# Performance work log

Hardware: AMD Instinct MI355X
Metric: run time of the kernel (lower is better)

## Reference

```python
import jax, jax.numpy as jnp
import numpy as np

V, E, H, T, B, A = 100000, 300, 256, 128, 64, 8
FH, NC = 256, 2
G = 2 * H  # gcn_input_dim = hidden_size * 2


def setup_inputs() -> dict:
    key = jax.random.key(0)
    ks = jax.random.split(key, 28)
    def n(k, shape, scale=0.05):
        return jax.random.normal(k, shape, dtype=jnp.float32) * scale
    return {
        "sentence": jax.random.randint(ks[0], (B, T), 0, V),
        "aspect": jax.random.randint(ks[1], (B, A), 0, V),
        "pos_class": jax.random.randint(ks[2], (B, T), 0, 18),
        "dep_tags": jax.random.randint(ks[3], (B, T), 0, 40),
        "text_len": jax.random.randint(ks[4], (B,), 1, T + 1),
        "aspect_len": jax.random.randint(ks[5], (B,), 1, A + 1),
        "dep_rels": jax.random.randint(ks[6], (B, T), 0, 40),
        "dep_heads": jax.random.randint(ks[7], (B, T), 0, T),
        "aspect_position": jax.random.randint(ks[8], (B, T), 0, 2),
        "dep_dirs": jax.random.randint(ks[9], (B, T), 0, 3),
        # frozen GloVe table
        "glove_emb": jax.random.normal(ks[10], (V, E), dtype=jnp.float32),
        # BiLSTM (1 layer): PyTorch layout, gates ordered i,f,g,o
        "w_ih_f": n(ks[11], (4 * H, E)), "w_hh_f": n(ks[12], (4 * H, H)),
        "b_ih_f": n(ks[13], (4 * H,)), "b_hh_f": n(ks[14], (4 * H,)),
        "w_ih_b": n(ks[15], (4 * H, E)), "w_hh_b": n(ks[16], (4 * H, H)),
        "b_ih_b": n(ks[17], (4 * H,)), "b_hh_b": n(ks[18], (4 * H,)),
        # 'gcn' attention branch: self.gat = nn.Linear(G, G)
        "gat_w": n(ks[19], (G, G)), "gat_b": n(ks[20], (G,)),
        # fcs MLP (num_mlps = 2)
        "fc1_w": n(ks[21], (FH, G)), "fc1_b": n(ks[22], (FH,)),
        "fc2_w": n(ks[23], (FH, FH)), "fc2_b": n(ks[24], (FH,)),
        "fcf_w": n(ks[25], (NC, FH)), "fcf_b": n(ks[26], (NC,)),
    }


def _lstm_dir(x, w_ih, w_hh, b_ih, b_hh, reverse):
    """One direction of a PyTorch-style LSTM. x: (B, T, E) -> (B, T, H)."""
    Bn = x.shape[0]
    Hh = w_hh.shape[1]
    xs = jnp.swapaxes(x, 0, 1)  # (T, B, E)
    if reverse:
        xs = xs[::-1]
    def step(carry, xt):
        h, c = carry
        g = xt @ w_ih.T + b_ih + h @ w_hh.T + b_hh  # (B, 4H)
        i, f, gg, o = jnp.split(g, 4, axis=-1)
        c = jax.nn.sigmoid(f) * c + jax.nn.sigmoid(i) * jnp.tanh(gg)
        h = jax.nn.sigmoid(o) * jnp.tanh(c)
        return (h, c), h
    init = (jnp.zeros((Bn, Hh), x.dtype), jnp.zeros((Bn, Hh), x.dtype))
    _, hs = jax.lax.scan(step, init, xs)
    if reverse:
        hs = hs[::-1]
    return jnp.swapaxes(hs, 0, 1)


def _bilstm(x, w_ih_f, w_hh_f, b_ih_f, b_hh_f, w_ih_b, w_hh_b, b_ih_b, b_hh_b):
    fwd = _lstm_dir(x, w_ih_f, w_hh_f, b_ih_f, b_hh_f, reverse=False)
    bwd = _lstm_dir(x, w_ih_b, w_hh_b, b_ih_b, b_hh_b, reverse=True)
    return jnp.concatenate([fwd, bwd], axis=-1)  # (B, T, 2H)


def reference(sentence, aspect, pos_class, dep_tags, text_len, aspect_len,
              dep_rels, dep_heads, aspect_position, dep_dirs,
              glove_emb, w_ih_f, w_hh_f, b_ih_f, b_hh_f,
              w_ih_b, w_hh_b, b_ih_b, b_hh_b,
              gat_w, gat_b, fc1_w, fc1_b, fc2_w, fc2_b, fcf_w, fcf_b):
    # fmask: per-token validity mask derived from text_len (inputs_to_deprel_adj)
    fmask = (jnp.arange(T)[None, :] < text_len[:, None]).astype(jnp.float32)  # (B, T)
    # embedding lookup (dropout is identity in eval mode)
    feature = glove_emb[sentence]  # (B, T, E)
    # BiLSTM over the sentence. (aspect branch is dead code in the 'gcn' path:
    # aspect_feature is computed but never used, so we omit it.)
    feature = _bilstm(feature, w_ih_f, w_hh_f, b_ih_f, b_hh_f,
                      w_ih_b, w_hh_b, b_ih_b, b_hh_b)  # (B, T, 2H)
    # 'gcn' branch: linear, mask, sum over tokens, relu
    gat_out = feature @ gat_w.T + gat_b           # (B, T, 2H)
    gat_out = gat_out * fmask[:, :, None]
    gat_out = jax.nn.relu(jnp.sum(gat_out, axis=1))  # (B, 2H)
    # fcs MLP + final classifier
    x = jax.nn.relu(gat_out @ fc1_w.T + fc1_b)
    x = jax.nn.relu(x @ fc2_w.T + fc2_b)
    logit = x @ fcf_w.T + fcf_b                    # (B, NC)
    return logit
```

## Files before the change

### kernel.cpp

```cpp
#include <hip/hip_runtime.h>
#include <hip/hip_bf16.h>
#include <math.h>

#define B_  64
#define T_  128
#define E_  300
#define H_  256
#define G4  1024
#define N2  2048
#define GG  512
#define FH_ 256
#define NC_ 2
#define KP  320

typedef __attribute__((ext_vector_type(8))) short short8;
typedef __attribute__((ext_vector_type(4))) float f32x4;
typedef unsigned short ushort_t;
typedef unsigned long long u64;

static __device__ __forceinline__ ushort_t bf16bits(float x) {
    __hip_bfloat16 b = __float2bfloat16(x);
    return __builtin_bit_cast(ushort_t, b);
}
static __device__ __forceinline__ float bf16lo(unsigned v) {
    return __builtin_bit_cast(float, v << 16);
}
static __device__ __forceinline__ float bf16hi(unsigned v) {
    return __builtin_bit_cast(float, v & 0xffff0000u);
}

static __device__ __forceinline__ float sigm_f(float x) {
    return __fdividef(1.f, 1.f + __expf(-x));
}
static __device__ __forceinline__ float tanh_f(float x) {
    return 1.f - __fdividef(2.f, __expf(2.f * x) + 1.f);
}

static __device__ __forceinline__ void ld8_sc0(const u64* p, u64 v[8]) {
    u64 r0, r1, r2, r3, r4, r5, r6, r7;
    asm volatile(
        "global_load_dwordx2 %0, %8, off sc0\n\t"
        "global_load_dwordx2 %1, %8, off offset:8 sc0\n\t"
        "global_load_dwordx2 %2, %8, off offset:16 sc0\n\t"
        "global_load_dwordx2 %3, %8, off offset:24 sc0\n\t"
        "global_load_dwordx2 %4, %8, off offset:32 sc0\n\t"
        "global_load_dwordx2 %5, %8, off offset:40 sc0\n\t"
        "global_load_dwordx2 %6, %8, off offset:48 sc0\n\t"
        "global_load_dwordx2 %7, %8, off offset:56 sc0\n\t"
        "s_waitcnt vmcnt(0)"
        : "=&v"(r0), "=&v"(r1), "=&v"(r2), "=&v"(r3),
          "=&v"(r4), "=&v"(r5), "=&v"(r6), "=&v"(r7)
        : "v"(p)
        : "memory");
    v[0] = r0; v[1] = r1; v[2] = r2; v[3] = r3;
    v[4] = r4; v[5] = r5; v[6] = r6; v[7] = r7;
}

#define OFF_BIAS  262144
#define OFF_WIH   524288
#define OFF_A     1835008
#define OFF_XEMB  2097152
#define OFF_XPROJ 8388608
#define OFF_S     41943040

__global__ __launch_bounds__(256) void k_prep(
    const int*   __restrict__ sentence,
    const float* __restrict__ glove,
    const float* __restrict__ w_ih_f,
    const float* __restrict__ w_ih_b,
    const float* __restrict__ b_ih_f, const float* __restrict__ b_hh_f,
    const float* __restrict__ b_ih_b, const float* __restrict__ b_hh_b,
    u64*         __restrict__ hbufB,
    u64*         __restrict__ hbufA,
    float*       __restrict__ bias2,
    ushort_t*    __restrict__ wihshuf,
    ushort_t*    __restrict__ xemb) {
    const int idx = blockIdx.x * 256 + threadIdx.x;

    if (idx < 16384) { hbufB[idx] = 0ull; hbufA[idx] = 0ull; }

    if (idx < N2) {
        bias2[idx] = (idx < G4) ? (b_ih_f[idx] + b_hh_f[idx])
                                : (b_ih_b[idx - G4] + b_hh_b[idx - G4]);
    }

    if (idx < 81920) {
        const int ntile = idx / 640;
        const int r     = idx % 640;
        const int ks    = r / 64;
        const int lane  = r % 64;
        const int n  = ntile * 16 + (lane & 15);
        const int k0 = ks * 32 + ((lane >> 4) << 3);
        const float* src = (n < G4) ? (w_ih_f + (size_t)n * E_)
                                    : (w_ih_b + (size_t)(n - G4) * E_);
        ushort_t o[8];
        #pragma unroll
        for (int j = 0; j < 8; ++j) {
            const int k = k0 + j;
            o[j] = (k < E_) ? bf16bits(src[k]) : (ushort_t)0;
        }
        uint4 pk;
        pk.x = (unsigned)o[0] | ((unsigned)o[1] << 16);
        pk.y = (unsigned)o[2] | ((unsigned)o[3] << 16);
        pk.z = (unsigned)o[4] | ((unsigned)o[5] << 16);
        pk.w = (unsigned)o[6] | ((unsigned)o[7] << 16);
        *(uint4*)(wihshuf + (size_t)idx * 8) = pk;
    }

    {
        const int m  = idx / 80;
        const int c4 = (idx % 80) * 4;
        const float* row = glove + (size_t)sentence[m] * E_;
        ushort_t o[4];
        #pragma unroll
        for (int j = 0; j < 4; ++j) {
            const int k = c4 + j;
            o[j] = (k < E_) ? bf16bits(row[k]) : (ushort_t)0;
        }
        uint2 pk;
        pk.x = (unsigned)o[0] | ((unsigned)o[1] << 16);
        pk.y = (unsigned)o[2] | ((unsigned)o[3] << 16);
        *(uint2*)(xemb + (size_t)m * KP + c4) = pk;
    }
}

__global__ __launch_bounds__(256) void k_xproj_mfma(
    const ushort_t* __restrict__ xemb,
    const ushort_t* __restrict__ wihshuf,
    const float*    __restrict__ bias2,
    ushort_t*       __restrict__ xprojb) {
    __shared__ ushort_t ct[4][16][136];
    const int tid = threadIdx.x;
    const int wave = tid >> 6, lane = tid & 63;
    const int quad = lane >> 4, l15 = lane & 15;
    const int m0 = blockIdx.x * 64 + wave * 16;
    const ushort_t* ap = xemb + (size_t)(m0 + l15) * KP;
    const ushort_t* wp = wihshuf + (size_t)blockIdx.y * 40960 + lane * 8;

    f32x4 acc[8] = {};
    #pragma unroll
    for (int ks = 0; ks < 10; ++ks) {
        short8 af = *(const short8*)(ap + ks * 32 + quad * 8);
        #pragma unroll
        for (int j = 0; j < 8; ++j) {
            short8 bf = *(const short8*)(wp + (size_t)(j * 10 + ks) * 512);
            acc[j] = __builtin_amdgcn_mfma_f32_16x16x32_bf16(af, bf, acc[j], 0, 0, 0);
        }
    }
    #pragma unroll
    for (int j = 0; j < 8; ++j) {
        const float bias = bias2[blockIdx.y * 128 + j * 16 + l15];
        #pragma unroll
        for (int r = 0; r < 4; ++r)
            ct[wave][quad * 4 + r][j * 16 + l15] = bf16bits(acc[j][r] + bias);
    }
    #pragma unroll
    for (int i = 0; i < 4; ++i) {
        const int row = i * 4 + (lane >> 4);
        uint4 v = *(const uint4*)&ct[wave][row][l15 * 8];
        *(uint4*)(xprojb + (size_t)(m0 + row) * N2 + blockIdx.y * 128 + l15 * 8) = v;
    }
}

__global__ __launch_bounds__(256, 1) void k_lstm_sync(
    const ushort_t* __restrict__ xprojb,
    const float*    __restrict__ w_hh_f,
    const float*    __restrict__ w_hh_b,
    const int*      __restrict__ text_len,
    u64*            __restrict__ hbufB,
    u64*            __restrict__ hbufA,
    float*          __restrict__ S)
{
    __shared__ ushort_t hl[16][264];
    __shared__ float    gLDS[4 * 16 * 33];

    const int tid   = threadIdx.x;
    const int g     = blockIdx.x & 7;
    const int slice = blockIdx.x >> 3;
    const int d     = g & 1;
    const int b0    = (g >> 1) * 16;
    const int j0    = slice * 32;
    const int wave  = tid >> 6, lane = tid & 63;
    const int quad  = lane >> 4, l15 = lane & 15;

    const float* whh = d ? w_hh_b : w_hh_f;
    u64* slabB0 = hbufB + (size_t)g * 2048;
    u64* slabB1 = hbufB + 16384 + (size_t)g * 2048;
    u64* slabA0 = hbufA + (size_t)g * 2048;
    u64* slabA1 = hbufA + 16384 + (size_t)g * 2048;

    short8 wfrag[2][8];
    #pragma unroll
    for (int u = 0; u < 2; ++u) {
        const int n = wave * 256 + j0 + u * 16 + l15;
        #pragma unroll
        for (int ks = 0; ks < 8; ++ks) {
            const float* p = whh + (size_t)n * 256 + ks * 32 + quad * 8;
            float4 lo = *(const float4*)p;
            float4 hi = *(const float4*)(p + 4);
            short8 f;
            f[0] = (short)bf16bits(lo.x); f[1] = (short)bf16bits(lo.y);
            f[2] = (short)bf16bits(lo.z); f[3] = (short)bf16bits(lo.w);
            f[4] = (short)bf16bits(hi.x); f[5] = (short)bf16bits(hi.y);
            f[6] = (short)bf16bits(hi.z); f[7] = (short)bf16bits(hi.w);
            wfrag[u][ks] = f;
        }
    }

    const int mb  = tid >> 4;
    const int pp0 = (tid & 15) * 8;
    const int wi  = mb * 128 + slice * 16 + (tid & 15);
    const int c0  = (tid & 15) * 2;
    const int lenm = text_len[b0 + mb];
    float cst0 = 0.f, cst1 = 0.f, s0 = 0.f, s1 = 0.f;
    bool slow = false;

    for (int t = 0; t < T_; ++t) {
        const int tt = d ? (T_ - 1 - t) : t;
        const ushort_t* xp = xprojb +
            ((size_t)(b0 + mb) * T_ + tt) * N2 + d * G4 + j0;
        const unsigned vi = *(const unsigned*)(xp + c0);
        const unsigned vf = *(const unsigned*)(xp + 256 + c0);
        const unsigned vg = *(const unsigned*)(xp + 512 + c0);
        const unsigned vo = *(const unsigned*)(xp + 768 + c0);

        const u64* srcA = ((t & 1) ? slabA1 : slabA0) + mb * 128 + pp0;
        const u64* srcB = ((t & 1) ? slabB1 : slabB0) + mb * 128 + pp0;
        u64 v[8];
        bool need = true;
        if (!slow) {
            for (int tries = 0; tries < 48 && need; ++tries) {
                ld8_sc0(srcA, v);
                bool ok = true;
                #pragma unroll
                for (int i = 0; i < 8; ++i)
                    ok = ok && ((unsigned)(v[i] >> 32) == (unsigned)t);
                if (ok) need = false;
            }
            if (need) slow = true;
        }
        if (need) {
            for (;;) {
                #pragma unroll
                for (int i = 0; i < 8; ++i)
                    v[i] = __hip_atomic_load(srcB + i, __ATOMIC_RELAXED,
                                             __HIP_MEMORY_SCOPE_AGENT);
                bool ok = true;
                #pragma unroll
                for (int i = 0; i < 8; ++i)
                    ok = ok && ((unsigned)(v[i] >> 32) == (unsigned)t);
                if (ok) break;
            }
        }
        {
            uint4 pk0, pk1;
            pk0.x = (unsigned)v[0]; pk0.y = (unsigned)v[1];
            pk0.z = (unsigned)v[2]; pk0.w = (unsigned)v[3];
            pk1.x = (unsigned)v[4]; pk1.y = (unsigned)v[5];
            pk1.z = (unsigned)v[6]; pk1.w = (unsigned)v[7];
            *(uint4*)&hl[mb][pp0 * 2]     = pk0;
            *(uint4*)&hl[mb][pp0 * 2 + 8] = pk1;
        }
        __syncthreads();

        short8 af[8];
        #pragma unroll
        for (int ks = 0; ks < 8; ++ks)
            af[ks] = *(const short8*)&hl[l15][ks * 32 + quad * 8];
        f32x4 acc[2] = {};
        #pragma unroll
        for (int ks = 0; ks < 8; ++ks) {
            acc[0] = __builtin_amdgcn_mfma_f32_16x16x32_bf16(
                af[ks], wfrag[0][ks], acc[0], 0, 0, 0);
            acc[1] = __builtin_amdgcn_mfma_f32_16x16x32_bf16(
                af[ks], wfrag[1][ks], acc[1], 0, 0, 0);
        }
        #pragma unroll
        for (int u = 0; u < 2; ++u)
            #pragma unroll
            for (int r = 0; r < 4; ++r)
                gLDS[wave * 528 + (quad * 4 + r) * 33 + u * 16 + l15] = acc[u][r];
        __syncthreads();

        const int gb = mb * 33 + c0;
        const float gi0 = gLDS[gb],        gi1 = gLDS[gb + 1];
        const float gf0 = gLDS[528 + gb],  gf1 = gLDS[528 + gb + 1];
        const float gg0 = gLDS[1056 + gb], gg1 = gLDS[1056 + gb + 1];
        const float go0 = gLDS[1584 + gb], go1 = gLDS[1584 + gb + 1];
        const float i0 = sigm_f(bf16lo(vi) + gi0);
        const float i1 = sigm_f(bf16hi(vi) + gi1);
        const float f0 = sigm_f(bf16lo(vf) + gf0);
        const float f1 = sigm_f(bf16hi(vf) + gf1);
        const float gc0 = tanh_f(bf16lo(vg) + gg0);
        const float gc1 = tanh_f(bf16hi(vg) + gg1);
        const float o0 = sigm_f(bf16lo(vo) + go0);
        const float o1 = sigm_f(bf16hi(vo) + go1);
        cst0 = f0 * cst0 + i0 * gc0;
        cst1 = f1 * cst1 + i1 * gc1;
        const float h0 = o0 * tanh_f(cst0);
        const float h1 = o1 * tanh_f(cst1);
        if (tt < lenm) { s0 += h0; s1 += h1; }

        const u64 word = ((u64)(unsigned)(t + 1) << 32) |
                         (u64)((unsigned)bf16bits(h0) |
                               ((unsigned)bf16bits(h1) << 16));
        u64* dstA = ((t & 1) ? slabA0 : slabA1) + wi;
        u64* dstB = ((t & 1) ? slabB0 : slabB1) + wi;
        *(volatile u64*)dstA = word;
        __hip_atomic_store(dstB, word, __ATOMIC_RELAXED,
                           __HIP_MEMORY_SCOPE_AGENT);
    }

    float2 sv; sv.x = s0; sv.y = s1;
    *(float2*)(S + (size_t)(b0 + mb) * GG + d * H_ + j0 + c0) = sv;
}

__global__ __launch_bounds__(256) void k_head(
    const float* __restrict__ S,
    const int*   __restrict__ text_len,
    const float* __restrict__ gat_w, const float* __restrict__ gat_b,
    const float* __restrict__ fc1_w, const float* __restrict__ fc1_b,
    const float* __restrict__ fc2_w, const float* __restrict__ fc2_b,
    const float* __restrict__ fcf_w, const float* __restrict__ fcf_b,
    float* __restrict__ out)
{
    __shared__ float sb[GG];
    __shared__ float x1[GG];
    __shared__ float x2[FH_];
    __shared__ float x3[FH_];
    const int b = blockIdx.x, tid = threadIdx.x;
    sb[tid]       = S[(size_t)b * GG + tid];
    sb[tid + 256] = S[(size_t)b * GG + tid + 256];
    __syncthreads();
    const float lenf = (float)text_len[b];
    #pragma unroll
    for (int r = 0; r < 2; ++r) {
        const int n = tid + r * 256;
        float acc = gat_b[n] * lenf;
        const float* w = gat_w + (size_t)n * GG;
        for (int k = 0; k < GG; ++k) acc += sb[k] * w[k];
        x1[n] = fmaxf(acc, 0.f);
    }
    __syncthreads();
    {
        float acc = fc1_b[tid];
        const float* w = fc1_w + (size_t)tid * GG;
        for (int k = 0; k < GG; ++k) acc += x1[k] * w[k];
        x2[tid] = fmaxf(acc, 0.f);
    }
    __syncthreads();
    {
        float acc = fc2_b[tid];
        const float* w = fc2_w + (size_t)tid * FH_;
        for (int k = 0; k < FH_; ++k) acc += x2[k] * w[k];
        x3[tid] = fmaxf(acc, 0.f);
    }
    __syncthreads();
    if (tid < NC_) {
        float acc = fcf_b[tid];
        const float* w = fcf_w + (size_t)tid * FH_;
        for (int k = 0; k < FH_; ++k) acc += x3[k] * w[k];
        out[b * NC_ + tid] = acc;
    }
}

extern "C" void kernel_launch(void* const* d_in, const int* in_sizes, int n_in,
                              void* d_out, int out_size, void* d_ws, size_t ws_size,
                              hipStream_t stream) {
    const int*   sentence = (const int*)  d_in[0];
    const int*   text_len = (const int*)  d_in[4];
    const float* glove    = (const float*)d_in[10];
    const float* w_ih_f   = (const float*)d_in[11];
    const float* w_hh_f   = (const float*)d_in[12];
    const float* b_ih_f   = (const float*)d_in[13];
    const float* b_hh_f   = (const float*)d_in[14];
    const float* w_ih_b   = (const float*)d_in[15];
    const float* w_hh_b   = (const float*)d_in[16];
    const float* b_ih_b   = (const float*)d_in[17];
    const float* b_hh_b   = (const float*)d_in[18];
    const float* gat_w    = (const float*)d_in[19];
    const float* gat_b    = (const float*)d_in[20];
    const float* fc1_w    = (const float*)d_in[21];
    const float* fc1_b    = (const float*)d_in[22];
    const float* fc2_w    = (const float*)d_in[23];
    const float* fc2_b    = (const float*)d_in[24];
    const float* fcf_w    = (const float*)d_in[25];
    const float* fcf_b    = (const float*)d_in[26];
    float* out = (float*)d_out;

    char* ws = (char*)d_ws;
    u64*      hbufB   = (u64*)ws;
    float*    bias2   = (float*)(ws + OFF_BIAS);
    ushort_t* wihshuf = (ushort_t*)(ws + OFF_WIH);
    u64*      hbufA   = (u64*)(ws + OFF_A);
    ushort_t* xemb    = (ushort_t*)(ws + OFF_XEMB);
    ushort_t* xprojb  = (ushort_t*)(ws + OFF_XPROJ);
    float*    S       = (float*)(ws + OFF_S);

    k_prep<<<2560, 256, 0, stream>>>(sentence, glove, w_ih_f, w_ih_b,
                                     b_ih_f, b_hh_f, b_ih_b, b_hh_b,
                                     hbufB, hbufA, bias2, wihshuf, xemb);
    dim3 gx(128, 16);
    k_xproj_mfma<<<gx, 256, 0, stream>>>(xemb, wihshuf, bias2, xprojb);
    k_lstm_sync<<<64, 256, 0, stream>>>(xprojb, w_hh_f, w_hh_b, text_len,
                                        hbufB, hbufA, S);
    k_head<<<64, 256, 0, stream>>>(S, text_len, gat_w, gat_b,
                                   fc1_w, fc1_b, fc2_w, fc2_b,
                                   fcf_w, fcf_b, out);
}
```

Measured before the change: 711.4 us.

## Map LSTM block groups onto the same XCD via atomic role assignment

Blocks of the recurrent LSTM kernel now read their XCC_ID and claim a (group, slice) role through atomic counters. The goal is for the 8 blocks that exchange hidden state every timestep to share one XCD and its L2, so the per-step cross-block handshake does not go through cross-die coherence. It adds a startup barrier across all 64 blocks and an overflow path for XCDs that receive more than 8 blocks. The prep kernel also zeroes the full double-buffered hidden-state area and the control counters.

```diff
diff --git a/kernel.cpp b/kernel.cpp
--- a/kernel.cpp
+++ b/kernel.cpp
@@ -57,6 +57,7 @@
 }
 
 #define OFF_BIAS  262144
+#define OFF_CTL   270336
 #define OFF_WIH   524288
 #define OFF_A     1835008
 #define OFF_XEMB  2097152
@@ -72,12 +73,14 @@
     const float* __restrict__ b_ih_b, const float* __restrict__ b_hh_b,
     u64*         __restrict__ hbufB,
     u64*         __restrict__ hbufA,
+    unsigned*    __restrict__ ctl,
     float*       __restrict__ bias2,
     ushort_t*    __restrict__ wihshuf,
     ushort_t*    __restrict__ xemb) {
     const int idx = blockIdx.x * 256 + threadIdx.x;
 
-    if (idx < 16384) { hbufB[idx] = 0ull; hbufA[idx] = 0ull; }
+    if (idx < 32768) { hbufB[idx] = 0ull; hbufA[idx] = 0ull; }
+    if (idx < 16) ctl[idx] = 0u;
 
     if (idx < N2) {
         bias2[idx] = (idx < G4) ? (b_ih_f[idx] + b_hh_f[idx])
@@ -169,14 +172,49 @@
     const int*      __restrict__ text_len,
     u64*            __restrict__ hbufB,
     u64*            __restrict__ hbufA,
+    unsigned*       __restrict__ ctl,
     float*          __restrict__ S)
 {
     __shared__ ushort_t hl[16][264];
     __shared__ float    gLDS[4 * 16 * 33];
+    __shared__ int      roleS[2];
 
     const int tid   = threadIdx.x;
-    const int g     = blockIdx.x & 7;
-    const int slice = blockIdx.x >> 3;
+
+    if (tid == 0) {
+        unsigned xcd;
+        asm volatile("s_getreg_b32 %0, hwreg(HW_REG_XCC_ID)" : "=s"(xcd));
+        xcd &= 7u;
+        const unsigned r = __hip_atomic_fetch_add(
+            &ctl[xcd], 1u, __ATOMIC_RELAXED, __HIP_MEMORY_SCOPE_AGENT);
+        __hip_atomic_fetch_add(&ctl[9], 1u, __ATOMIC_RELAXED,
+                               __HIP_MEMORY_SCOPE_AGENT);
+        while (__hip_atomic_load(&ctl[9], __ATOMIC_RELAXED,
+                                 __HIP_MEMORY_SCOPE_AGENT) < 64u) {}
+        unsigned slot;
+        if (r < 8u) {
+            slot = xcd * 8u + r;
+        } else {
+            const unsigned ov = __hip_atomic_fetch_add(
+                &ctl[8], 1u, __ATOMIC_RELAXED, __HIP_MEMORY_SCOPE_AGENT);
+            unsigned c = 0, found = 63;
+            for (unsigned x = 0; x < 8u; ++x) {
+                unsigned cnt = __hip_atomic_load(&ctl[x], __ATOMIC_RELAXED,
+                                                 __HIP_MEMORY_SCOPE_AGENT);
+                unsigned cap = cnt < 8u ? cnt : 8u;
+                unsigned fre = 8u - cap;
+                if (ov < c + fre) { found = x * 8u + cap + (ov - c); break; }
+                c += fre;
+            }
+            slot = found;
+        }
+        roleS[0] = (int)(slot >> 3);
+        roleS[1] = (int)(slot & 7u);
+    }
+    __syncthreads();
+    const int g     = roleS[0];
+    const int slice = roleS[1];
+
     const int d     = g & 1;
     const int b0    = (g >> 1) * 16;
     const int j0    = slice * 32;
@@ -391,6 +429,7 @@
     char* ws = (char*)d_ws;
     u64*      hbufB   = (u64*)ws;
     float*    bias2   = (float*)(ws + OFF_BIAS);
+    unsigned* ctl     = (unsigned*)(ws + OFF_CTL);
     ushort_t* wihshuf = (ushort_t*)(ws + OFF_WIH);
     u64*      hbufA   = (u64*)(ws + OFF_A);
     ushort_t* xemb    = (ushort_t*)(ws + OFF_XEMB);
@@ -399,11 +438,11 @@
 
     k_prep<<<2560, 256, 0, stream>>>(sentence, glove, w_ih_f, w_ih_b,
                                      b_ih_f, b_hh_f, b_ih_b, b_hh_b,
-                                     hbufB, hbufA, bias2, wihshuf, xemb);
+                                     hbufB, hbufA, ctl, bias2, wihshuf, xemb);
     dim3 gx(128, 16);
     k_xproj_mfma<<<gx, 256, 0, stream>>>(xemb, wihshuf, bias2, xprojb);
     k_lstm_sync<<<64, 256, 0, stream>>>(xprojb, w_hh_f, w_hh_b, text_len,
-                                        hbufB, hbufA, S);
+                                        hbufB, hbufA, ctl, S);
     k_head<<<64, 256, 0, stream>>>(S, text_len, gat_w, gat_b,
                                    fc1_w, fc1_b, fc2_w, fc2_b,
                                    fcf_w, fcf_b, out);
```

After: 710.7 us. Within noise of the previous version (-0.1%).
